# Performance work log

Hardware: AMD Instinct MI355X
Metric: run time of the kernel (lower is better)

The kernel has to match this reference:

```python
import jax, jax.numpy as jnp
import numpy as np

H = 16
QK_DIM = 1024
EPS = 1e-5


def setup_inputs() -> dict:
    key = jax.random.key(0)
    ks = jax.random.split(key, 5)
    B, N, M, D = 2, 2048, 2048, 1024
    x = jax.random.normal(ks[0], (B, N, D), jnp.float32)
    context = jax.random.normal(ks[1], (B, M, D), jnp.float32)
    Wq = jax.random.normal(ks[2], (QK_DIM, D), jnp.float32) * (D ** -0.5)
    Wkv = jax.random.normal(ks[3], (QK_DIM + 1024, D), jnp.float32) * (D ** -0.5)
    Wtalk = jax.random.normal(ks[4], (H, H), jnp.float32) * (H ** -0.5)
    ln_gamma = jnp.ones((H,), jnp.float32)
    ln_beta = jnp.zeros((H,), jnp.float32)
    return {"x": x, "context": context, "Wq": Wq, "Wkv": Wkv,
            "Wtalk": Wtalk, "ln_gamma": ln_gamma, "ln_beta": ln_beta}


def _split_heads(t):
    # b n (h d) -> b h n d
    b, n, hd = t.shape
    return t.reshape(b, n, H, hd // H).transpose(0, 2, 1, 3)


def reference(x, context, Wq, Wkv, Wtalk, ln_gamma, ln_beta):
    q = x @ Wq.T                      # [B,N,QK]
    kv = context @ Wkv.T              # [B,M,QK+V]
    k, v = kv[..., :QK_DIM], kv[..., QK_DIM:]
    q, k, v = _split_heads(q), _split_heads(k), _split_heads(v)
    q = q * (q.shape[-1] ** -0.5)
    scores = jnp.einsum('bhid,bhjd->bhij', q, k)          # [B,H,N,M]
    aw = jax.nn.softmax(scores, axis=-1)
    # talking heads: Linear over head axis then LayerNorm over head axis
    aw = jnp.einsum('bhij,gh->bgij', aw, Wtalk)
    mu = jnp.mean(aw, axis=1, keepdims=True)
    var = jnp.var(aw, axis=1, keepdims=True)
    aw = (aw - mu) * jax.lax.rsqrt(var + EPS)
    aw = aw * ln_gamma[None, :, None, None] + ln_beta[None, :, None, None]
    attn = jnp.einsum('bhij,bhjd->bhid', aw, v)           # [B,H,N,dv]
    b, h, n, d = attn.shape
    return attn.transpose(0, 2, 1, 3).reshape(b, n, h * d)  # [B,N,V]
```

## Files before the change

### kernel.cpp

```cpp
#include <hip/hip_runtime.h>


typedef __attribute__((ext_vector_type(8))) short short8;
typedef __attribute__((ext_vector_type(4))) short short4v;
typedef __attribute__((ext_vector_type(4))) float float4v;
typedef unsigned short u16;

#define MFMA16(a, b, c) __builtin_amdgcn_mfma_f32_16x16x32_bf16((a), (b), (c), 0, 0, 0)

__device__ inline u16 f2bf(float f) {
  unsigned u = __float_as_uint(f);
  u += 0x7FFFu + ((u >> 16) & 1u);
  return (u16)(u >> 16);
}

__global__ __launch_bounds__(256) void cast_bf16(const float* __restrict__ in,
                                                 u16* __restrict__ out, int n) {
  int i = (blockIdx.x * 256 + threadIdx.x) * 8;
  if (i + 8 > n) return;
  float4v f0 = *(const float4v*)(in + i);
  float4v f1 = *(const float4v*)(in + i + 4);
  short8 o;
  o[0] = (short)f2bf(f0[0]); o[1] = (short)f2bf(f0[1]);
  o[2] = (short)f2bf(f0[2]); o[3] = (short)f2bf(f0[3]);
  o[4] = (short)f2bf(f1[0]); o[5] = (short)f2bf(f1[1]);
  o[6] = (short)f2bf(f1[2]); o[7] = (short)f2bf(f1[3]);
  *(short8*)(out + i) = o;
}

template <int MODE>
__global__ __launch_bounds__(256, 4) void gemm_bt(const u16* __restrict__ A,
                                                  const u16* __restrict__ W,
                                                  u16* __restrict__ out0,
                                                  u16* __restrict__ out1) {
  __shared__ u16 As[64][40];
  __shared__ u16 Ws[64][40];
  const int t = threadIdx.x;
  const int wave = t >> 6, l = t & 63, l15 = l & 15, lq = l >> 4;
  const int r0 = blockIdx.x * 64, c0 = blockIdx.y * 64;
  const int srow = t >> 2, sch = t & 3;
  const u16* ag = A + (r0 + srow) * 1024 + sch * 8;
  const u16* wg = W + (c0 + srow) * 1024 + sch * 8;

  float4v acc[4];
#pragma unroll
  for (int i = 0; i < 4; ++i) acc[i] = (float4v){0.f, 0.f, 0.f, 0.f};

  short8 av = *(const short8*)ag;
  short8 wv = *(const short8*)wg;
  for (int kt = 0; kt < 32; ++kt) {
    __syncthreads();
    *(short8*)&As[srow][sch * 8] = av;
    *(short8*)&Ws[srow][sch * 8] = wv;
    __syncthreads();
    if (kt < 31) {
      av = *(const short8*)(ag + (kt + 1) * 32);
      wv = *(const short8*)(wg + (kt + 1) * 32);
    }
    short8 af = *(const short8*)&As[wave * 16 + l15][lq * 8];
#pragma unroll
    for (int fn = 0; fn < 4; ++fn) {
      short8 bf = *(const short8*)&Ws[fn * 16 + l15][lq * 8];
      acc[fn] = MFMA16(af, bf, acc[fn]);
    }
  }
#pragma unroll
  for (int fn = 0; fn < 4; ++fn) {
#pragma unroll
    for (int r = 0; r < 4; ++r) {
      int row = r0 + wave * 16 + lq * 4 + r;
      int col = c0 + fn * 16 + l15;
      int b = row >> 11, n = row & 2047;
      float v = acc[fn][r];
      if (MODE == 0) {
        v *= 0.125f;
        int h = col >> 6, d = col & 63;
        out0[(((b * 16 + h) * 2048 + n) << 6) + d] = f2bf(v);
      } else {
        if (col < 1024) {
          int h = col >> 6, d = col & 63;
          out0[(((b * 16 + h) * 2048 + n) << 6) + d] = f2bf(v);
        } else {
          int cc = col - 1024;
          int h = cc >> 6, d = cc & 63;
          out1[(((b * 16 + h) * 2048 + n) << 6) + d] = f2bf(v);
        }
      }
    }
  }
}

__global__ __launch_bounds__(256) void transpose_v(const u16* __restrict__ vh,
                                                   u16* __restrict__ vt) {
  __shared__ u16 tile[64][72];
  const int t = threadIdx.x;
  const int j0 = blockIdx.x * 64, h = blockIdx.y, b = blockIdx.z;
  const u16* src = vh + (((b * 16 + h) * 2048 + j0) << 6);
  int row = t >> 2, c = t & 3;
  short8 v0 = *(const short8*)(src + row * 64 + c * 8);
  short8 v1 = *(const short8*)(src + row * 64 + (c + 4) * 8);
  *(short8*)&tile[row][c * 8] = v0;
  *(short8*)&tile[row][(c + 4) * 8] = v1;
  __syncthreads();
  int d = t >> 2, jc = t & 3;
  short8 o0, o1;
#pragma unroll
  for (int jj = 0; jj < 8; ++jj) o0[jj] = (short)tile[jc * 16 + jj][d];
#pragma unroll
  for (int jj = 0; jj < 8; ++jj) o1[jj] = (short)tile[jc * 16 + 8 + jj][d];
  u16* dst = vt + ((b * 16 + h) * 64 + d) * 2048 + j0 + jc * 16;
  *(short8*)dst = o0;
  *(short8*)(dst + 8) = o1;
}

__global__ __launch_bounds__(1024) void attn_fused(
    const u16* __restrict__ qh, const u16* __restrict__ kh,
    const u16* __restrict__ vt, const float* __restrict__ wtalk,
    const float* __restrict__ gamma, const float* __restrict__ beta,
    float* __restrict__ out) {
  __shared__ u16 P_lds[2][512 * 36];
  __shared__ u16 Y_lds[2][16 * 16 * 36];

  const int tid = threadIdx.x;
  const int wv = tid >> 6;
  const int l = tid & 63, l15 = l & 15, lq = l >> 4;
  const int i0 = blockIdx.x * 16;
  const int b = blockIdx.y;
  const int bh = b * 16 + wv;

  {
    u16* pz = &P_lds[0][0];
    for (int z = tid; z < 2 * 512 * 36; z += 1024) pz[z] = 0;
  }

  short8 wfrag;
#pragma unroll
  for (int t8 = 0; t8 < 8; ++t8) {
    int h = lq * 8 + t8;
    float wval = (h < 16) ? wtalk[l15 * 16 + h] : 0.f;
    wfrag[t8] = (short)f2bf(wval);
  }
  float gam[4], bet[4];
#pragma unroll
  for (int r = 0; r < 4; ++r) {
    gam[r] = gamma[lq * 4 + r];
    bet[r] = beta[lq * 4 + r];
  }

  const u16* qbase = qh + ((bh * 2048 + i0) << 6);
  short8 qf0 = *(const short8*)(qbase + l15 * 64 + lq * 8);
  short8 qf1 = *(const short8*)(qbase + l15 * 64 + 32 + lq * 8);
  const u16* kbase = kh + ((bh * 2048) << 6);
  const u16* vbase = vt + (bh * 64) * 2048;

  __syncthreads();

  float ps0 = 0.f, ps1 = 0.f, ps2 = 0.f, ps3 = 0.f;
  short8 k00 = *(const short8*)(kbase + l15 * 64 + lq * 8);
  short8 k01 = *(const short8*)(kbase + l15 * 64 + 32 + lq * 8);
  short8 k10 = *(const short8*)(kbase + (16 + l15) * 64 + lq * 8);
  short8 k11 = *(const short8*)(kbase + (16 + l15) * 64 + 32 + lq * 8);
  for (int jt = 0; jt < 64; ++jt) {
    short8 n00, n01, n10, n11;
    if (jt < 63) {
      const u16* kp = kbase + (((jt + 1) * 32) << 6);
      n00 = *(const short8*)(kp + l15 * 64 + lq * 8);
      n01 = *(const short8*)(kp + l15 * 64 + 32 + lq * 8);
      n10 = *(const short8*)(kp + (16 + l15) * 64 + lq * 8);
      n11 = *(const short8*)(kp + (16 + l15) * 64 + 32 + lq * 8);
    }
    float4v s0 = {0.f, 0.f, 0.f, 0.f}, s1 = {0.f, 0.f, 0.f, 0.f};
    s0 = MFMA16(qf0, k00, s0);
    s0 = MFMA16(qf1, k01, s0);
    s1 = MFMA16(qf0, k10, s1);
    s1 = MFMA16(qf1, k11, s1);
    ps0 += __expf(s0[0]) + __expf(s1[0]);
    ps1 += __expf(s0[1]) + __expf(s1[1]);
    ps2 += __expf(s0[2]) + __expf(s1[2]);
    ps3 += __expf(s0[3]) + __expf(s1[3]);
    k00 = n00; k01 = n01; k10 = n10; k11 = n11;
  }
#pragma unroll
  for (int d = 1; d < 16; d <<= 1) {
    ps0 += __shfl_xor(ps0, d);
    ps1 += __shfl_xor(ps1, d);
    ps2 += __shfl_xor(ps2, d);
    ps3 += __shfl_xor(ps3, d);
  }
  float bc[4];
  bc[0] = -logf(ps0); bc[1] = -logf(ps1);
  bc[2] = -logf(ps2); bc[3] = -logf(ps3);

  float4v acc0 = {0.f, 0.f, 0.f, 0.f}, acc1 = acc0, acc2 = acc0, acc3 = acc0;
  short8 kc00 = *(const short8*)(kbase + l15 * 64 + lq * 8);
  short8 kc01 = *(const short8*)(kbase + l15 * 64 + 32 + lq * 8);
  short8 kc10 = *(const short8*)(kbase + (16 + l15) * 64 + lq * 8);
  short8 kc11 = *(const short8*)(kbase + (16 + l15) * 64 + 32 + lq * 8);
  short8 v0, v1, v2, v3;

  for (int jt = 0; jt <= 64; ++jt) {
    const int buf = jt & 1, pbuf = (jt - 1) & 1;
    if (jt >= 1) {
      const u16* vp = vbase + (jt - 1) * 32 + lq * 8;
      v0 = *(const short8*)(vp + (l15) * 2048);
      v1 = *(const short8*)(vp + (16 + l15) * 2048);
      v2 = *(const short8*)(vp + (32 + l15) * 2048);
      v3 = *(const short8*)(vp + (48 + l15) * 2048);
    }
    short8 kn00, kn01, kn10, kn11;
    if (jt + 1 < 64) {
      const u16* kp = kbase + (((jt + 1) * 32) << 6);
      kn00 = *(const short8*)(kp + l15 * 64 + lq * 8);
      kn01 = *(const short8*)(kp + l15 * 64 + 32 + lq * 8);
      kn10 = *(const short8*)(kp + (16 + l15) * 64 + lq * 8);
      kn11 = *(const short8*)(kp + (16 + l15) * 64 + 32 + lq * 8);
    }
    if (jt < 64) {
      float4v s0 = {0.f, 0.f, 0.f, 0.f}, s1 = {0.f, 0.f, 0.f, 0.f};
      s0 = MFMA16(qf0, kc00, s0);
      s0 = MFMA16(qf1, kc01, s0);
      s1 = MFMA16(qf0, kc10, s1);
      s1 = MFMA16(qf1, kc11, s1);
      int ebase = (lq * 4) * 32 + l15;
#pragma unroll
      for (int r = 0; r < 4; ++r) {
        float p0 = __expf(s0[r] + bc[r]);
        float p1 = __expf(s1[r] + bc[r]);
        P_lds[buf][(ebase + r * 32) * 36 + wv] = f2bf(p0);
        P_lds[buf][(ebase + r * 32 + 16) * 36 + wv] = f2bf(p1);
      }
    }
    __syncthreads();
    if (jt < 64) {
      float4v t0 = {0.f, 0.f, 0.f, 0.f}, t1 = {0.f, 0.f, 0.f, 0.f};
      {
        int e00 = wv * 32 + l15;
        int e10 = wv * 32 + 16 + l15;
        const u16* p0p = &P_lds[buf][e00 * 36 + lq * 8];
        const u16* p1p = &P_lds[buf][e10 * 36 + lq * 8];
        short4v x0 = *(const short4v*)p0p;
        short4v x1 = *(const short4v*)(p0p + 4);
        short4v y0 = *(const short4v*)p1p;
        short4v y1 = *(const short4v*)(p1p + 4);
        short8 pb0 = __builtin_shufflevector(x0, x1, 0, 1, 2, 3, 4, 5, 6, 7);
        short8 pb1 = __builtin_shufflevector(y0, y1, 0, 1, 2, 3, 4, 5, 6, 7);
        t0 = MFMA16(wfrag, pb0, t0);
        t1 = MFMA16(wfrag, pb1, t1);
      }
#pragma unroll
      for (int c2 = 0; c2 < 2; ++c2) {
        float4v tt = c2 ? t1 : t0;
        float sum = tt[0] + tt[1] + tt[2] + tt[3];
        sum += __shfl_xor(sum, 16);
        sum += __shfl_xor(sum, 32);
        float mu = sum * 0.0625f;
        float ss = tt[0] * tt[0] + tt[1] * tt[1] + tt[2] * tt[2] + tt[3] * tt[3];
        ss += __shfl_xor(ss, 16);
        ss += __shfl_xor(ss, 32);
        float var = ss * 0.0625f - mu * mu;
        float rs = rsqrtf(var + 1e-5f);
#pragma unroll
        for (int r = 0; r < 4; ++r) {
          float y = (tt[r] - mu) * rs * gam[r] + bet[r];
          Y_lds[buf][((lq * 4 + r) * 16 + wv) * 36 + c2 * 16 + l15] = f2bf(y);
        }
      }
    }
    if (jt >= 1) {
      short8 yf = *(const short8*)&Y_lds[pbuf][(wv * 16 + l15) * 36 + lq * 8];
      acc0 = MFMA16(yf, v0, acc0);
      acc1 = MFMA16(yf, v1, acc1);
      acc2 = MFMA16(yf, v2, acc2);
      acc3 = MFMA16(yf, v3, acc3);
    }
    kc00 = kn00; kc01 = kn01; kc10 = kn10; kc11 = kn11;
  }
  float* ob = out + (b * 2048 + i0) * 1024 + wv * 64;
#pragma unroll
  for (int r = 0; r < 4; ++r) {
    float* orow = ob + (lq * 4 + r) * 1024;
    orow[l15] = acc0[r];
    orow[16 + l15] = acc1[r];
    orow[32 + l15] = acc2[r];
    orow[48 + l15] = acc3[r];
  }
}

extern "C" void kernel_launch(void* const* d_in, const int* in_sizes, int n_in,
                              void* d_out, int out_size, void* d_ws,
                              size_t ws_size, hipStream_t stream) {
  const float* x = (const float*)d_in[0];
  const float* ctx = (const float*)d_in[1];
  const float* Wq = (const float*)d_in[2];
  const float* Wkv = (const float*)d_in[3];
  const float* Wtalk = (const float*)d_in[4];
  const float* gam = (const float*)d_in[5];
  const float* bet = (const float*)d_in[6];
  float* out = (float*)d_out;

  u16* xb = (u16*)d_ws;
  u16* cb = xb + 4194304;
  u16* wqb = cb + 4194304;
  u16* wkvb = wqb + 1048576;
  u16* qhb = wkvb + 2097152;
  u16* khb = qhb + 4194304;
  u16* vhb = khb + 4194304;
  u16* vtb = vhb + 4194304;

  cast_bf16<<<2048, 256, 0, stream>>>(x, xb, 4194304);
  cast_bf16<<<2048, 256, 0, stream>>>(ctx, cb, 4194304);
  cast_bf16<<<512, 256, 0, stream>>>(Wq, wqb, 1048576);
  cast_bf16<<<1024, 256, 0, stream>>>(Wkv, wkvb, 2097152);

  gemm_bt<0><<<dim3(64, 16), 256, 0, stream>>>(xb, wqb, qhb, nullptr);
  gemm_bt<1><<<dim3(64, 32), 256, 0, stream>>>(cb, wkvb, khb, vhb);

  transpose_v<<<dim3(32, 16, 2), 256, 0, stream>>>(vhb, vtb);

  attn_fused<<<dim3(128, 2), 1024, 0, stream>>>(qhb, khb, vtb, Wtalk, gam, bet,
                                                out);
}
```

Baseline: 506.7 us.

## Split fused attention into QK-exp, talking-heads LN, and PV kernels via workspace

Replaces the single fused attention kernel, which launches only 256 blocks, with three kernels when the workspace is large enough. The first computes QK^T and exp and stores unnormalised bf16 probabilities, with row sums accumulated atomically. The second normalises, applies the talking-heads mix and the LayerNorm in place. The third does the PV matmul. This gains parallelism and simpler per-kernel work at the cost of writing and re-reading a 256MB probability tensor through HBM. Softmax skips max subtraction, so exp could overflow for large scores.

```diff
diff --git a/kernel.cpp b/kernel.cpp
--- a/kernel.cpp
+++ b/kernel.cpp
@@ -5,6 +5,7 @@
 typedef __attribute__((ext_vector_type(4))) short short4v;
 typedef __attribute__((ext_vector_type(4))) float float4v;
 typedef unsigned short u16;
+typedef unsigned int u32;
 
 #define MFMA16(a, b, c) __builtin_amdgcn_mfma_f32_16x16x32_bf16((a), (b), (c), 0, 0, 0)
 
@@ -12,6 +13,10 @@
   unsigned u = __float_as_uint(f);
   u += 0x7FFFu + ((u >> 16) & 1u);
   return (u16)(u >> 16);
+}
+__device__ inline float bf2f(u16 v) {
+  u32 u = ((u32)v) << 16;
+  return __uint_as_float(u);
 }
 
 __global__ __launch_bounds__(256) void cast_bf16(const float* __restrict__ in,
@@ -113,6 +118,183 @@
   *(short8*)(dst + 8) = o1;
 }
 
+__global__ __launch_bounds__(256) void qk_exp(const u16* __restrict__ qh,
+                                              const u16* __restrict__ kh,
+                                              u16* __restrict__ pt,
+                                              float* __restrict__ lsum) {
+  __shared__ u16 stage[16 * 1160];
+  const int tid = threadIdx.x, wv = tid >> 6, l = tid & 63;
+  const int l15 = l & 15, lq = l >> 4;
+  const int i0 = blockIdx.x * 16, j0 = blockIdx.y * 64, b = blockIdx.z;
+  const int hbase = wv * 4;
+
+  short8 qf[4][2];
+#pragma unroll
+  for (int hh = 0; hh < 4; ++hh) {
+    const u16* qp = qh + (((b * 16 + hbase + hh) * 2048 + i0 + l15) << 6) + lq * 8;
+    qf[hh][0] = *(const short8*)qp;
+    qf[hh][1] = *(const short8*)(qp + 32);
+  }
+  float4v acc[4][4];
+#pragma unroll
+  for (int hh = 0; hh < 4; ++hh)
+#pragma unroll
+    for (int jf = 0; jf < 4; ++jf) acc[hh][jf] = (float4v){0.f, 0.f, 0.f, 0.f};
+
+#pragma unroll
+  for (int hh = 0; hh < 4; ++hh) {
+    const u16* kr = kh + (((b * 16 + hbase + hh) * 2048 + j0) << 6);
+#pragma unroll
+    for (int jf = 0; jf < 4; ++jf) {
+      const u16* kp = kr + ((jf * 16 + l15) << 6) + lq * 8;
+      short8 k0 = *(const short8*)kp;
+      short8 k1 = *(const short8*)(kp + 32);
+      acc[hh][jf] = MFMA16(qf[hh][0], k0, acc[hh][jf]);
+      acc[hh][jf] = MFMA16(qf[hh][1], k1, acc[hh][jf]);
+    }
+  }
+#pragma unroll
+  for (int hh = 0; hh < 4; ++hh) {
+    float rsum[4] = {0.f, 0.f, 0.f, 0.f};
+#pragma unroll
+    for (int jf = 0; jf < 4; ++jf)
+#pragma unroll
+      for (int r = 0; r < 4; ++r) {
+        float e = __expf(acc[hh][jf][r]);
+        rsum[r] += e;
+        stage[(hbase + hh) * 1160 + (lq * 4 + r) * 72 + jf * 16 + l15] = f2bf(e);
+      }
+#pragma unroll
+    for (int r = 0; r < 4; ++r) {
+      float v = rsum[r];
+      v += __shfl_xor(v, 1);
+      v += __shfl_xor(v, 2);
+      v += __shfl_xor(v, 4);
+      v += __shfl_xor(v, 8);
+      if (l15 == 0)
+        unsafeAtomicAdd(&lsum[((b * 2048) + i0 + lq * 4 + r) * 16 + hbase + hh], v);
+    }
+  }
+  __syncthreads();
+  const int h = tid >> 4, ii = tid & 15;
+  const u16* src = &stage[h * 1160 + ii * 72];
+  u16* dst = pt + ((size_t)((b * 128 + blockIdx.x) * 32 + blockIdx.y)) * 16384 +
+             h * 1024 + ii * 64;
+#pragma unroll
+  for (int q = 0; q < 8; ++q) *(short8*)(dst + q * 8) = *(const short8*)(src + q * 8);
+}
+
+__global__ __launch_bounds__(256) void talk_ln(u16* __restrict__ pt,
+                                               const float* __restrict__ lsum,
+                                               const float* __restrict__ wtalk,
+                                               const float* __restrict__ gamma,
+                                               const float* __restrict__ beta) {
+  __shared__ float rl[256];
+  const int tid = threadIdx.x;
+  const int i0 = blockIdx.x * 16, b = blockIdx.z;
+  rl[(tid & 15) * 16 + (tid >> 4)] =
+      1.0f / lsum[((b * 2048) + i0 + (tid & 15)) * 16 + (tid >> 4)];
+  __syncthreads();
+
+  const int i = tid >> 4, jq = tid & 15;
+  u16* tp = pt + ((size_t)((b * 128 + blockIdx.x) * 32 + blockIdx.y)) * 16384 +
+            i * 64 + jq * 4;
+  short4v raw[16];
+#pragma unroll
+  for (int h = 0; h < 16; ++h) raw[h] = *(const short4v*)(tp + h * 1024);
+
+#pragma unroll
+  for (int p = 0; p < 2; ++p) {
+    float ph[16][2];
+#pragma unroll
+    for (int h = 0; h < 16; ++h) {
+      float s = rl[i * 16 + h];
+      ph[h][0] = bf2f((u16)raw[h][p * 2]) * s;
+      ph[h][1] = bf2f((u16)raw[h][p * 2 + 1]) * s;
+    }
+    float y[16][2];
+#pragma unroll
+    for (int g = 0; g < 16; ++g) {
+      float s0 = 0.f, s1 = 0.f;
+#pragma unroll
+      for (int h = 0; h < 16; ++h) {
+        float w = wtalk[g * 16 + h];
+        s0 += w * ph[h][0];
+        s1 += w * ph[h][1];
+      }
+      y[g][0] = s0;
+      y[g][1] = s1;
+    }
+    float mu0 = 0.f, mu1 = 0.f;
+#pragma unroll
+    for (int g = 0; g < 16; ++g) { mu0 += y[g][0]; mu1 += y[g][1]; }
+    mu0 *= 0.0625f;
+    mu1 *= 0.0625f;
+    float v0 = 0.f, v1 = 0.f;
+#pragma unroll
+    for (int g = 0; g < 16; ++g) {
+      float d0 = y[g][0] - mu0, d1 = y[g][1] - mu1;
+      v0 += d0 * d0;
+      v1 += d1 * d1;
+    }
+    float rs0 = rsqrtf(v0 * 0.0625f + 1e-5f);
+    float rs1 = rsqrtf(v1 * 0.0625f + 1e-5f);
+#pragma unroll
+    for (int g = 0; g < 16; ++g) {
+      float a0 = (y[g][0] - mu0) * rs0 * gamma[g] + beta[g];
+      float a1 = (y[g][1] - mu1) * rs1 * gamma[g] + beta[g];
+      u32 pk = (u32)f2bf(a0) | ((u32)f2bf(a1) << 16);
+      *(u32*)(tp + g * 1024 + p * 2) = pk;
+    }
+  }
+}
+
+__global__ __launch_bounds__(256) void pv(const u16* __restrict__ yt,
+                                          const u16* __restrict__ vt,
+                                          float* __restrict__ out) {
+  const int tid = threadIdx.x, wv = tid >> 6, l = tid & 63;
+  const int l15 = l & 15, lq = l >> 4;
+  const int b = blockIdx.z, h = blockIdx.y, it = blockIdx.x * 4 + wv;
+  const u16* yb = yt + ((size_t)((b * 128 + it) * 32)) * 16384 + h * 1024 +
+                  l15 * 64 + lq * 8;
+  const u16* vb = vt + ((b * 16 + h) * 64) * 2048 + lq * 8;
+  float4v acc[4];
+#pragma unroll
+  for (int d = 0; d < 4; ++d) acc[d] = (float4v){0.f, 0.f, 0.f, 0.f};
+
+  short8 a = *(const short8*)yb;
+  short8 v0 = *(const short8*)(vb + l15 * 2048);
+  short8 v1 = *(const short8*)(vb + (16 + l15) * 2048);
+  short8 v2 = *(const short8*)(vb + (32 + l15) * 2048);
+  short8 v3 = *(const short8*)(vb + (48 + l15) * 2048);
+  for (int s = 0; s < 64; ++s) {
+    short8 an, n0, n1, n2, n3;
+    if (s < 63) {
+      int sn = s + 1;
+      an = *(const short8*)(yb + (sn >> 1) * 16384 + (sn & 1) * 32);
+      const u16* vp = vb + sn * 32;
+      n0 = *(const short8*)(vp + l15 * 2048);
+      n1 = *(const short8*)(vp + (16 + l15) * 2048);
+      n2 = *(const short8*)(vp + (32 + l15) * 2048);
+      n3 = *(const short8*)(vp + (48 + l15) * 2048);
+    }
+    acc[0] = MFMA16(a, v0, acc[0]);
+    acc[1] = MFMA16(a, v1, acc[1]);
+    acc[2] = MFMA16(a, v2, acc[2]);
+    acc[3] = MFMA16(a, v3, acc[3]);
+    a = an; v0 = n0; v1 = n1; v2 = n2; v3 = n3;
+  }
+  float* ob = out + (b * 2048 + it * 16 + lq * 4) * 1024 + h * 64;
+#pragma unroll
+  for (int r = 0; r < 4; ++r) {
+    float* orow = ob + r * 1024;
+    orow[l15] = acc[0][r];
+    orow[16 + l15] = acc[1][r];
+    orow[32 + l15] = acc[2][r];
+    orow[48 + l15] = acc[3][r];
+  }
+}
+
 __global__ __launch_bounds__(1024) void attn_fused(
     const u16* __restrict__ qh, const u16* __restrict__ kh,
     const u16* __restrict__ vt, const float* __restrict__ wtalk,
@@ -132,7 +314,6 @@
     u16* pz = &P_lds[0][0];
     for (int z = tid; z < 2 * 512 * 36; z += 1024) pz[z] = 0;
   }
-
   short8 wfrag;
 #pragma unroll
   for (int t8 = 0; t8 < 8; ++t8) {
@@ -146,7 +327,6 @@
     gam[r] = gamma[lq * 4 + r];
     bet[r] = beta[lq * 4 + r];
   }
-
   const u16* qbase = qh + ((bh * 2048 + i0) << 6);
   short8 qf0 = *(const short8*)(qbase + l15 * 64 + lq * 8);
   short8 qf1 = *(const short8*)(qbase + l15 * 64 + 32 + lq * 8);
@@ -306,6 +486,10 @@
   u16* khb = qhb + 4194304;
   u16* vhb = khb + 4194304;
   u16* vtb = vhb + 4194304;
+  u16* ptb = vtb + 4194304;
+  float* lsum = (float*)(ptb + 134217728);
+
+  const size_t NEED = 56623104ull + 268435456ull + 262144ull;
 
   cast_bf16<<<2048, 256, 0, stream>>>(x, xb, 4194304);
   cast_bf16<<<2048, 256, 0, stream>>>(ctx, cb, 4194304);
@@ -317,6 +501,13 @@
 
   transpose_v<<<dim3(32, 16, 2), 256, 0, stream>>>(vhb, vtb);
 
-  attn_fused<<<dim3(128, 2), 1024, 0, stream>>>(qhb, khb, vtb, Wtalk, gam, bet,
-                                                out);
-}
+  if (ws_size >= NEED) {
+    hipMemsetAsync(lsum, 0, 262144, stream);
+    qk_exp<<<dim3(128, 32, 2), 256, 0, stream>>>(qhb, khb, ptb, lsum);
+    talk_ln<<<dim3(128, 32, 2), 256, 0, stream>>>(ptb, lsum, Wtalk, gam, bet);
+    pv<<<dim3(32, 16, 2), 256, 0, stream>>>(ptb, vtb, out);
+  } else {
+    attn_fused<<<dim3(128, 2), 1024, 0, stream>>>(qhb, khb, vtb, Wtalk, gam,
+                                                  bet, out);
+  }
+}
```

Result: no change. 508.7 us (+0.4%).
